# Kernel optimization log

Hardware: AMD Instinct MI355X
Metric: run time of the kernel (lower is better)

The kernel has to match this reference:

```python
import jax, jax.numpy as jnp
import numpy as np

D_MODEL = 1024
N_HEADS = 16
HEAD_DIM = D_MODEL // N_HEADS
D_FF = 4096
EPS = 1e-5


def setup_inputs() -> dict:
    key = jax.random.key(0)
    ks = jax.random.split(key, 12)
    s = 0.02
    return {
        "x": jax.random.normal(ks[0], (2, 2048, D_MODEL), jnp.float32),
        "wq": jax.random.normal(ks[1], (D_MODEL, D_MODEL), jnp.float32) * s,
        "bq": jnp.zeros((D_MODEL,), jnp.float32),
        "wk": jax.random.normal(ks[2], (D_MODEL, D_MODEL), jnp.float32) * s,
        "bk": jnp.zeros((D_MODEL,), jnp.float32),
        "wv": jax.random.normal(ks[3], (D_MODEL, D_MODEL), jnp.float32) * s,
        "bv": jnp.zeros((D_MODEL,), jnp.float32),
        "wo": jax.random.normal(ks[4], (D_MODEL, D_MODEL), jnp.float32) * s,
        "bo": jnp.zeros((D_MODEL,), jnp.float32),
        "w1": jax.random.normal(ks[5], (D_MODEL, D_FF), jnp.float32) * s,
        "b1": jnp.zeros((D_FF,), jnp.float32),
        "w2": jax.random.normal(ks[6], (D_FF, D_MODEL), jnp.float32) * s,
        "b2": jnp.zeros((D_MODEL,), jnp.float32),
        "g1": jnp.ones((D_MODEL,), jnp.float32),
        "be1": jnp.zeros((D_MODEL,), jnp.float32),
        "g2": jnp.ones((D_MODEL,), jnp.float32),
        "be2": jnp.zeros((D_MODEL,), jnp.float32),
    }


def _layer_norm(x, g, b):
    mu = jnp.mean(x, axis=-1, keepdims=True)
    var = jnp.var(x, axis=-1, keepdims=True)
    return (x - mu) * jax.lax.rsqrt(var + EPS) * g + b


def reference(x, wq, bq, wk, bk, wv, bv, wo, bo, w1, b1, w2, b2, g1, be1, g2, be2):
    B, S, D = x.shape
    nx = _layer_norm(x, g1, be1)
    # projections -> [B, H, S, d]
    def split_heads(t):
        return t.reshape(B, S, N_HEADS, HEAD_DIM).transpose(0, 2, 1, 3)
    q = split_heads(nx @ wq + bq)
    k = split_heads(nx @ wk + bk)
    v = split_heads(nx @ wv + bv)
    scores = jnp.einsum("bhqd,bhkd->bhqk", q, k) / jnp.sqrt(jnp.float32(HEAD_DIM))
    attn = jax.nn.softmax(scores, axis=-1)
    out = jnp.einsum("bhqk,bhkd->bhqd", attn, v)
    out = out.transpose(0, 2, 1, 3).reshape(B, S, D)
    x = x + (out @ wo + bo)
    nx = _layer_norm(x, g2, be2)
    ff = jax.nn.relu(nx @ w1 + b1) @ w2 + b2
    return x + ff
```

## Files before the change

kernel.cpp:

```cpp
#include <hip/hip_runtime.h>


typedef __attribute__((ext_vector_type(8))) unsigned short u16x8;
typedef __attribute__((ext_vector_type(4))) unsigned short u16x4;
typedef __attribute__((ext_vector_type(8))) __bf16 bf16x8;
typedef __attribute__((ext_vector_type(4))) float f32x4;

#define C_SCALE 0.1803368801111f

static __device__ __forceinline__ unsigned short f2b(float f) {
    return __builtin_bit_cast(unsigned short, (__bf16)f);
}
static __device__ __forceinline__ float b2f(unsigned short h) {
    unsigned u = ((unsigned)h) << 16;
    float f;
    __builtin_memcpy(&f, &u, 4);
    return f;
}

static __device__ __forceinline__ void async_cp16(
    const unsigned short* g, unsigned short* l)
{
    __builtin_amdgcn_global_load_lds(
        (const __attribute__((address_space(1))) unsigned int*)g,
        (__attribute__((address_space(3))) unsigned int*)l,
        16, 0, 0);
}

__global__ __launch_bounds__(256) void transpose_all_k(
    const float* __restrict__ wq, const float* __restrict__ wk,
    const float* __restrict__ wv, const float* __restrict__ wo,
    const float* __restrict__ w1, const float* __restrict__ w2,
    unsigned short* __restrict__ wqkvT, unsigned short* __restrict__ woT,
    unsigned short* __restrict__ w1T, unsigned short* __restrict__ w2T)
{
    __shared__ unsigned short tile[32][33];
    const int ti = blockIdx.x;
    const float* in;
    unsigned short* out;
    int R, C, bi, bj;
    float sc = 1.0f;
    if (ti < 4096) {
        R = 1024; C = 1024;
        bi = (ti & 1023) >> 5; bj = ti & 31;
        int z = ti >> 10;
        in = (z == 0) ? wq : (z == 1) ? wk : (z == 2) ? wv : wo;
        out = (z < 3) ? wqkvT + (size_t)z * 1024 * 1024 : woT;
        if (z == 1) sc = C_SCALE;
    } else if (ti < 8192) {
        R = 1024; C = 4096;
        int l = ti - 4096;
        bi = l >> 7; bj = l & 127;
        in = w1; out = w1T;
    } else {
        R = 4096; C = 1024;
        int l = ti - 8192;
        bi = l >> 5; bj = l & 31;
        in = w2; out = w2T;
    }
    const int tx = threadIdx.x & 31, ty = threadIdx.x >> 5;
#pragma unroll
    for (int rr = 0; rr < 4; ++rr) {
        int r = ty + rr * 8;
        tile[r][tx] = f2b(in[(size_t)(bi * 32 + r) * C + bj * 32 + tx] * sc);
    }
    __syncthreads();
#pragma unroll
    for (int rr = 0; rr < 4; ++rr) {
        int r = ty + rr * 8;
        out[(size_t)(bj * 32 + r) * R + bi * 32 + tx] = tile[tx][r];
    }
}

__global__ __launch_bounds__(256) void concat3_k(
    const float* __restrict__ a, const float* __restrict__ b,
    const float* __restrict__ c, float* __restrict__ o)
{
    int t = blockIdx.x * 256 + threadIdx.x;
    float v = (t < 1024) ? a[t]
            : ((t < 2048) ? b[t - 1024] * C_SCALE : c[t - 2048]);
    o[t] = v;
}

__global__ __launch_bounds__(256) void ln_kernel(
    const float* __restrict__ x, const float* __restrict__ g,
    const float* __restrict__ be, unsigned short* __restrict__ o)
{
    const int row = blockIdx.x;
    const int t = threadIdx.x;
    const float* xr = x + (size_t)row * 1024;
    float4 v4 = *reinterpret_cast<const float4*>(&xr[t * 4]);
    float f[4] = {v4.x, v4.y, v4.z, v4.w};
    float s = f[0] + f[1] + f[2] + f[3];
    float ss = f[0] * f[0] + f[1] * f[1] + f[2] * f[2] + f[3] * f[3];
#pragma unroll
    for (int d = 1; d < 64; d <<= 1) {
        s += __shfl_xor(s, d);
        ss += __shfl_xor(ss, d);
    }
    __shared__ float sb[4], ssb[4];
    const int wave = t >> 6;
    if ((t & 63) == 0) { sb[wave] = s; ssb[wave] = ss; }
    __syncthreads();
    s = sb[0] + sb[1] + sb[2] + sb[3];
    ss = ssb[0] + ssb[1] + ssb[2] + ssb[3];
    const float mu = s * (1.0f / 1024.0f);
    const float var = ss * (1.0f / 1024.0f) - mu * mu;
    const float rs = rsqrtf(var + 1e-5f);
    u16x4 r4;
#pragma unroll
    for (int j = 0; j < 4; ++j)
        r4[j] = f2b((f[j] - mu) * rs * g[t * 4 + j] + be[t * 4 + j]);
    *reinterpret_cast<u16x4*>(&o[(size_t)row * 1024 + t * 4]) = r4;
}

__global__ __launch_bounds__(256) void reduce_ln_kernel(
    const unsigned short* __restrict__ pa, const unsigned short* __restrict__ pb,
    const float* __restrict__ bias, const float* __restrict__ x,
    const float* __restrict__ g, const float* __restrict__ be,
    float* __restrict__ x2, unsigned short* __restrict__ o)
{
    const int row = blockIdx.x;
    const int t = threadIdx.x;
    const size_t base = (size_t)row * 1024 + t * 4;
    float4 x4 = *reinterpret_cast<const float4*>(&x[base]);
    float4 bb = *reinterpret_cast<const float4*>(&bias[t * 4]);
    float f[4] = {x4.x + bb.x, x4.y + bb.y, x4.z + bb.z, x4.w + bb.w};
#pragma unroll
    for (int z = 0; z < 2; ++z) {
        u16x4 va = *reinterpret_cast<const u16x4*>(&pa[(size_t)z * 4096 * 1024 + base]);
        u16x4 vb = *reinterpret_cast<const u16x4*>(&pb[(size_t)z * 4096 * 1024 + base]);
#pragma unroll
        for (int j = 0; j < 4; ++j) f[j] += b2f(va[j]) + b2f(vb[j]);
    }
    *reinterpret_cast<float4*>(&x2[base]) = {f[0], f[1], f[2], f[3]};
    float s = f[0] + f[1] + f[2] + f[3];
    float ss = f[0] * f[0] + f[1] * f[1] + f[2] * f[2] + f[3] * f[3];
#pragma unroll
    for (int d = 1; d < 64; d <<= 1) {
        s += __shfl_xor(s, d);
        ss += __shfl_xor(ss, d);
    }
    __shared__ float sb[4], ssb[4];
    const int wave = t >> 6;
    if ((t & 63) == 0) { sb[wave] = s; ssb[wave] = ss; }
    __syncthreads();
    s = sb[0] + sb[1] + sb[2] + sb[3];
    ss = ssb[0] + ssb[1] + ssb[2] + ssb[3];
    const float mu = s * (1.0f / 1024.0f);
    const float var = ss * (1.0f / 1024.0f) - mu * mu;
    const float rs = rsqrtf(var + 1e-5f);
    u16x4 r4;
#pragma unroll
    for (int j = 0; j < 4; ++j)
        r4[j] = f2b((f[j] - mu) * rs * g[t * 4 + j] + be[t * 4 + j]);
    *reinterpret_cast<u16x4*>(&o[base]) = r4;
}

__global__ __launch_bounds__(256) void reduce_out4_k(
    const unsigned short* __restrict__ pa, const unsigned short* __restrict__ pb,
    const float* __restrict__ bias, const float* __restrict__ x2,
    float* __restrict__ out)
{
    const size_t i4 = ((size_t)blockIdx.x * 256 + threadIdx.x) * 4;
    float4 x4 = *reinterpret_cast<const float4*>(&x2[i4]);
    float4 bb = *reinterpret_cast<const float4*>(&bias[i4 & 1023]);
    float a0 = x4.x + bb.x, a1 = x4.y + bb.y, a2 = x4.z + bb.z, a3 = x4.w + bb.w;
#pragma unroll
    for (int z = 0; z < 2; ++z) {
        u16x4 va = *reinterpret_cast<const u16x4*>(&pa[(size_t)z * 4096 * 1024 + i4]);
        u16x4 vb = *reinterpret_cast<const u16x4*>(&pb[(size_t)z * 4096 * 1024 + i4]);
        a0 += b2f(va[0]) + b2f(vb[0]);
        a1 += b2f(va[1]) + b2f(vb[1]);
        a2 += b2f(va[2]) + b2f(vb[2]);
        a3 += b2f(va[3]) + b2f(vb[3]);
    }
    *reinterpret_cast<float4*>(&out[i4]) = {a0, a1, a2, a3};
}

template<int MODE, int RELU>
__global__ __launch_bounds__(256, 4) void gemm_bt(
    const unsigned short* __restrict__ A, int lda,
    const unsigned short* __restrict__ Bt, int ldb,
    const float* __restrict__ bias,
    void* __restrict__ Cv, void* __restrict__ Cv2, int N, int Kloop)
{
    __shared__ unsigned short As[128 * 32];
    __shared__ unsigned short Bs[128 * 32];
    const int t = threadIdx.x;
    const int wave = t >> 6, lane = t & 63;
    const int quad = lane >> 4, l16 = lane & 15;
    const int wm = wave >> 1, wn = wave & 1;
    const int m0 = blockIdx.y * 128;
    const int n0 = blockIdx.x * 128;
    const int k0 = blockIdx.z * Kloop;
    const int rl = lane >> 2;
    const int cl = (lane & 3) * 8;

    f32x4 acc[4][4];
#pragma unroll
    for (int mi = 0; mi < 4; ++mi)
#pragma unroll
        for (int ni = 0; ni < 4; ++ni) acc[mi][ni] = {0.f, 0.f, 0.f, 0.f};

    for (int kt = 0; kt < Kloop; kt += 32) {
#pragma unroll
        for (int j = 0; j < 4; ++j) {
            int c = wave * 4 + j;
            if (c < 8) {
                async_cp16(&A[(size_t)(m0 + c * 16 + rl) * lda + k0 + kt + cl],
                           &As[c * 512 + lane * 8]);
            } else {
                int bc = c - 8;
                async_cp16(&Bt[(size_t)(n0 + bc * 16 + rl) * ldb + k0 + kt + cl],
                           &Bs[bc * 512 + lane * 8]);
            }
        }
        __syncthreads();
        bf16x8 af[4], bfr[4];
#pragma unroll
        for (int mi = 0; mi < 4; ++mi)
            af[mi] = __builtin_bit_cast(bf16x8,
                *reinterpret_cast<const u16x8*>(&As[(wm * 64 + mi * 16 + l16) * 32 + quad * 8]));
#pragma unroll
        for (int ni = 0; ni < 4; ++ni)
            bfr[ni] = __builtin_bit_cast(bf16x8,
                *reinterpret_cast<const u16x8*>(&Bs[(wn * 64 + ni * 16 + l16) * 32 + quad * 8]));
#pragma unroll
        for (int mi = 0; mi < 4; ++mi)
#pragma unroll
            for (int ni = 0; ni < 4; ++ni)
                acc[mi][ni] = __builtin_amdgcn_mfma_f32_16x16x32_bf16(
                    af[mi], bfr[ni], acc[mi][ni], 0, 0, 0);
        __syncthreads();
    }

#pragma unroll
    for (int mi = 0; mi < 4; ++mi) {
        const int gr0 = m0 + wm * 64 + mi * 16 + quad * 4;
#pragma unroll
        for (int ni = 0; ni < 4; ++ni) {
            const int gc = n0 + wn * 64 + ni * 16 + l16;
            if (MODE == 2) {
                const float bv = bias[gc];
                if (gc < 2048) {
#pragma unroll
                    for (int r = 0; r < 4; ++r)
                        ((unsigned short*)Cv)[(size_t)(gr0 + r) * 2048 + gc] =
                            f2b(acc[mi][ni][r] + bv);
                } else {
                    u16x4 pk;
#pragma unroll
                    for (int r = 0; r < 4; ++r) pk[r] = f2b(acc[mi][ni][r] + bv);
                    const int b = gr0 >> 11, s0 = gr0 & 2047;
                    *reinterpret_cast<u16x4*>(
                        &((unsigned short*)Cv2)[((size_t)b * 1024 + (gc - 2048)) * 2048 + s0]) = pk;
                }
            } else if (MODE == 5) {
                unsigned short* base = (blockIdx.z < 2)
                    ? (unsigned short*)Cv  + (size_t)blockIdx.z * 4096 * N
                    : (unsigned short*)Cv2 + (size_t)(blockIdx.z - 2) * 4096 * N;
#pragma unroll
                for (int r = 0; r < 4; ++r)
                    base[(size_t)(gr0 + r) * N + gc] = f2b(acc[mi][ni][r]);
            } else {
                const float bv = bias[gc];
#pragma unroll
                for (int r = 0; r < 4; ++r) {
                    float v = acc[mi][ni][r] + bv;
                    if (RELU) v = fmaxf(v, 0.f);
                    ((unsigned short*)Cv)[(size_t)(gr0 + r) * N + gc] = f2b(v);
                }
            }
        }
    }
}

__global__ __launch_bounds__(256, 2) void attn_kernel(
    const unsigned short* __restrict__ qkb, const unsigned short* __restrict__ vbT,
    unsigned short* __restrict__ ao)
{
    __shared__ unsigned short Ks[64][72];
    __shared__ unsigned short Vt[64][72];
    __shared__ unsigned short Ps[4][32][72];
    const int t = threadIdx.x;
    const int wave = t >> 6, lane = t & 63;
    const int quad = lane >> 4, l16 = lane & 15;
    const int bh = blockIdx.y;
    const int b = bh >> 4, h = bh & 15;
    const int q0 = blockIdx.x * 128 + wave * 32;
    const size_t qk_base = (size_t)b * 2048 * 2048;
    const size_t vt_base = (size_t)b * 1024 * 2048 + (size_t)h * 64 * 2048;

    bf16x8 qf[2][2];
#pragma unroll
    for (int m = 0; m < 2; ++m)
#pragma unroll
        for (int kk = 0; kk < 2; ++kk)
            qf[m][kk] = __builtin_bit_cast(bf16x8, *reinterpret_cast<const u16x8*>(
                &qkb[qk_base + (size_t)(q0 + m * 16 + l16) * 2048 + h * 64 + kk * 32 + quad * 8]));

    u16x8 ones_u;
#pragma unroll
    for (int j = 0; j < 8; ++j) ones_u[j] = 0x3F80;
    const bf16x8 onesf = __builtin_bit_cast(bf16x8, ones_u);

    f32x4 o_acc[2][4], l_frag[2];
#pragma unroll
    for (int m = 0; m < 2; ++m) {
        l_frag[m] = {0.f, 0.f, 0.f, 0.f};
#pragma unroll
        for (int nf = 0; nf < 4; ++nf) o_acc[m][nf] = {0.f, 0.f, 0.f, 0.f};
    }

    const int srow0 = t >> 3, sc8 = (t & 7) * 8;
    const int srow1 = srow0 + 32;

    u16x8 kr[2], vr[2];
    kr[0] = *reinterpret_cast<const u16x8*>(&qkb[qk_base + (size_t)srow0 * 2048 + 1024 + h * 64 + sc8]);
    kr[1] = *reinterpret_cast<const u16x8*>(&qkb[qk_base + (size_t)srow1 * 2048 + 1024 + h * 64 + sc8]);
    vr[0] = *reinterpret_cast<const u16x8*>(&vbT[vt_base + (size_t)srow0 * 2048 + sc8]);
    vr[1] = *reinterpret_cast<const u16x8*>(&vbT[vt_base + (size_t)srow1 * 2048 + sc8]);

    for (int it = 0; it < 32; ++it) {
        __syncthreads();
        *reinterpret_cast<u16x8*>(&Ks[srow0][sc8]) = kr[0];
        *reinterpret_cast<u16x8*>(&Ks[srow1][sc8]) = kr[1];
        *reinterpret_cast<u16x8*>(&Vt[srow0][sc8]) = vr[0];
        *reinterpret_cast<u16x8*>(&Vt[srow1][sc8]) = vr[1];
        __syncthreads();
        if (it + 1 < 32) {
            const int ktn = (it + 1) * 64;
            kr[0] = *reinterpret_cast<const u16x8*>(&qkb[qk_base + (size_t)(ktn + srow0) * 2048 + 1024 + h * 64 + sc8]);
            kr[1] = *reinterpret_cast<const u16x8*>(&qkb[qk_base + (size_t)(ktn + srow1) * 2048 + 1024 + h * 64 + sc8]);
            vr[0] = *reinterpret_cast<const u16x8*>(&vbT[vt_base + (size_t)srow0 * 2048 + ktn + sc8]);
            vr[1] = *reinterpret_cast<const u16x8*>(&vbT[vt_base + (size_t)srow1 * 2048 + ktn + sc8]);
        }

#pragma unroll
        for (int kf = 0; kf < 4; ++kf) {
            bf16x8 kfr0 = __builtin_bit_cast(bf16x8,
                *reinterpret_cast<const u16x8*>(&Ks[kf * 16 + l16][quad * 8]));
            bf16x8 kfr1 = __builtin_bit_cast(bf16x8,
                *reinterpret_cast<const u16x8*>(&Ks[kf * 16 + l16][32 + quad * 8]));
#pragma unroll
            for (int m = 0; m < 2; ++m) {
                f32x4 s = {0.f, 0.f, 0.f, 0.f};
                s = __builtin_amdgcn_mfma_f32_16x16x32_bf16(kfr0, qf[m][0], s, 0, 0, 0);
                s = __builtin_amdgcn_mfma_f32_16x16x32_bf16(kfr1, qf[m][1], s, 0, 0, 0);
                unsigned lo = (unsigned)f2b(exp2f(s[0])) | ((unsigned)f2b(exp2f(s[1])) << 16);
                unsigned hi = (unsigned)f2b(exp2f(s[2])) | ((unsigned)f2b(exp2f(s[3])) << 16);
                *reinterpret_cast<uint2*>(&Ps[wave][m * 16 + l16][kf * 16 + quad * 4]) =
                    make_uint2(lo, hi);
            }
        }
#pragma unroll
        for (int kh = 0; kh < 2; ++kh) {
            bf16x8 pfr[2];
#pragma unroll
            for (int m = 0; m < 2; ++m)
                pfr[m] = __builtin_bit_cast(bf16x8,
                    *reinterpret_cast<const u16x8*>(&Ps[wave][m * 16 + l16][kh * 32 + quad * 8]));
#pragma unroll
            for (int m = 0; m < 2; ++m)
                l_frag[m] = __builtin_amdgcn_mfma_f32_16x16x32_bf16(
                    pfr[m], onesf, l_frag[m], 0, 0, 0);
#pragma unroll
            for (int nf = 0; nf < 4; ++nf) {
                bf16x8 vfr = __builtin_bit_cast(bf16x8,
                    *reinterpret_cast<const u16x8*>(&Vt[nf * 16 + l16][kh * 32 + quad * 8]));
#pragma unroll
                for (int m = 0; m < 2; ++m)
                    o_acc[m][nf] = __builtin_amdgcn_mfma_f32_16x16x32_bf16(
                        pfr[m], vfr, o_acc[m][nf], 0, 0, 0);
            }
        }
    }

#pragma unroll
    for (int m = 0; m < 2; ++m) {
#pragma unroll
        for (int r = 0; r < 4; ++r) {
            const float inv = 1.0f / l_frag[m][r];
            const int row = q0 + m * 16 + quad * 4 + r;
#pragma unroll
            for (int nf = 0; nf < 4; ++nf)
                ao[(size_t)b * 2048 * 1024 + (size_t)row * 1024 + h * 64 + nf * 16 + l16] =
                    f2b(o_acc[m][nf][r] * inv);
        }
    }
}

extern "C" void kernel_launch(void* const* d_in, const int* in_sizes, int n_in,
                              void* d_out, int out_size, void* d_ws, size_t ws_size,
                              hipStream_t stream)
{
    const float* x   = (const float*)d_in[0];
    const float* wq  = (const float*)d_in[1];
    const float* bq  = (const float*)d_in[2];
    const float* wk  = (const float*)d_in[3];
    const float* bk  = (const float*)d_in[4];
    const float* wv  = (const float*)d_in[5];
    const float* bv  = (const float*)d_in[6];
    const float* wo  = (const float*)d_in[7];
    const float* bo  = (const float*)d_in[8];
    const float* w1  = (const float*)d_in[9];
    const float* b1  = (const float*)d_in[10];
    const float* w2  = (const float*)d_in[11];
    const float* b2  = (const float*)d_in[12];
    const float* g1  = (const float*)d_in[13];
    const float* be1 = (const float*)d_in[14];
    const float* g2  = (const float*)d_in[15];
    const float* be2 = (const float*)d_in[16];
    float* out = (float*)d_out;
    char*  ws  = (char*)d_ws;

    const int M = 4096, D = 1024, DFF = 4096;
    const size_t MB = 1 << 20;

    unsigned short* wqkvT = (unsigned short*)(ws + 0 * MB);
    unsigned short* woT   = (unsigned short*)(ws + 6 * MB);
    unsigned short* w1T   = (unsigned short*)(ws + 8 * MB);
    unsigned short* w2T   = (unsigned short*)(ws + 16 * MB);
    unsigned short* ln    = (unsigned short*)(ws + 24 * MB);
    unsigned short* qkb   = (unsigned short*)(ws + 32 * MB);
    unsigned short* vbT   = (unsigned short*)(ws + 48 * MB);
    unsigned short* ao    = (unsigned short*)(ws + 56 * MB);
    unsigned short* ff1   = (unsigned short*)(ws + 32 * MB);
    float*          x2    = (float*)(ws + 64 * MB);
    float*          bqkv  = (float*)(ws + 80 * MB);
    unsigned short* pHi   = (unsigned short*)(ws + 80 * MB);
    unsigned short* pOlo  = (unsigned short*)(ws + 32 * MB);
    unsigned short* pFlo  = (unsigned short*)(ws + 0 * MB);

    transpose_all_k<<<12288, 256, 0, stream>>>(wq, wk, wv, wo, w1, w2,
                                               wqkvT, woT, w1T, w2T);
    concat3_k<<<12, 256, 0, stream>>>(bq, bk, bv, bqkv);
    ln_kernel<<<M, 256, 0, stream>>>(x, g1, be1, ln);
    gemm_bt<2, 0><<<dim3(24, 32), 256, 0, stream>>>(
        ln, D, wqkvT, D, bqkv, qkb, vbT, 3072, D);
    attn_kernel<<<dim3(16, 32), 256, 0, stream>>>(qkb, vbT, ao);
    gemm_bt<5, 0><<<dim3(8, 32, 4), 256, 0, stream>>>(
        ao, D, woT, D, nullptr, pHi, pOlo, 1024, 256);
    reduce_ln_kernel<<<M, 256, 0, stream>>>(pHi, pOlo, bo, x, g2, be2, x2, ln);
    gemm_bt<0, 1><<<dim3(32, 32), 256, 0, stream>>>(
        ln, D, w1T, D, b1, ff1, nullptr, DFF, D);
    gemm_bt<5, 0><<<dim3(8, 32, 4), 256, 0, stream>>>(
        ff1, DFF, w2T, DFF, nullptr, pHi, pFlo, 1024, 1024);
    reduce_out4_k<<<4096, 256, 0, stream>>>(pHi, pFlo, b2, x2, out);
}
```

Baseline: 375.5 us.

## Double-buffer K/V tiles and pass P fragments via permlane swaps instead of LDS

The attention kernel now double-buffers the K and V shared-memory tiles and prefetches two tiles ahead, so each iteration needs one barrier instead of two. The softmax probabilities are no longer round-tripped through a per-wave shared buffer. They are rearranged in registers with v_permlane32_swap/v_permlane16_swap, turning the MFMA accumulator layout directly into the A-operand layout for the PV product. This removes LDS traffic and waits on the P path at the cost of more shared memory for K/V, extra live registers, and reliance on gfx950-specific permlane instructions whose lane mapping must be exactly right.

```diff
diff --git a/kernel.cpp b/kernel.cpp
--- a/kernel.cpp
+++ b/kernel.cpp
@@ -5,6 +5,7 @@
 typedef __attribute__((ext_vector_type(4))) unsigned short u16x4;
 typedef __attribute__((ext_vector_type(8))) __bf16 bf16x8;
 typedef __attribute__((ext_vector_type(4))) float f32x4;
+typedef __attribute__((ext_vector_type(4))) unsigned int u32x4;
 
 #define C_SCALE 0.1803368801111f
 
@@ -280,12 +281,12 @@
     const unsigned short* __restrict__ qkb, const unsigned short* __restrict__ vbT,
     unsigned short* __restrict__ ao)
 {
-    __shared__ unsigned short Ks[64][72];
-    __shared__ unsigned short Vt[64][72];
-    __shared__ unsigned short Ps[4][32][72];
+    __shared__ unsigned short Ks[2][64][72];
+    __shared__ unsigned short Vt[2][64][72];
     const int t = threadIdx.x;
-    const int wave = t >> 6, lane = t & 63;
+    const int lane = t & 63;
     const int quad = lane >> 4, l16 = lane & 15;
+    const int wave = t >> 6;
     const int bh = blockIdx.y;
     const int b = bh >> 4, h = bh & 15;
     const int q0 = blockIdx.x * 128 + wave * 32;
@@ -316,65 +317,91 @@
     const int srow0 = t >> 3, sc8 = (t & 7) * 8;
     const int srow1 = srow0 + 32;
 
+    const unsigned short* kg0 = &qkb[qk_base + (size_t)srow0 * 2048 + 1024 + h * 64 + sc8];
+    const unsigned short* kg1 = kg0 + (size_t)32 * 2048;
+    const unsigned short* vg0 = &vbT[vt_base + (size_t)srow0 * 2048 + sc8];
+    const unsigned short* vg1 = vg0 + (size_t)32 * 2048;
+
     u16x8 kr[2], vr[2];
-    kr[0] = *reinterpret_cast<const u16x8*>(&qkb[qk_base + (size_t)srow0 * 2048 + 1024 + h * 64 + sc8]);
-    kr[1] = *reinterpret_cast<const u16x8*>(&qkb[qk_base + (size_t)srow1 * 2048 + 1024 + h * 64 + sc8]);
-    vr[0] = *reinterpret_cast<const u16x8*>(&vbT[vt_base + (size_t)srow0 * 2048 + sc8]);
-    vr[1] = *reinterpret_cast<const u16x8*>(&vbT[vt_base + (size_t)srow1 * 2048 + sc8]);
+    kr[0] = *reinterpret_cast<const u16x8*>(kg0);
+    kr[1] = *reinterpret_cast<const u16x8*>(kg1);
+    vr[0] = *reinterpret_cast<const u16x8*>(vg0);
+    vr[1] = *reinterpret_cast<const u16x8*>(vg1);
+    *reinterpret_cast<u16x8*>(&Ks[0][srow0][sc8]) = kr[0];
+    *reinterpret_cast<u16x8*>(&Ks[0][srow1][sc8]) = kr[1];
+    *reinterpret_cast<u16x8*>(&Vt[0][srow0][sc8]) = vr[0];
+    *reinterpret_cast<u16x8*>(&Vt[0][srow1][sc8]) = vr[1];
+    kr[0] = *reinterpret_cast<const u16x8*>(kg0 + (size_t)64 * 2048);
+    kr[1] = *reinterpret_cast<const u16x8*>(kg1 + (size_t)64 * 2048);
+    vr[0] = *reinterpret_cast<const u16x8*>(vg0 + 64);
+    vr[1] = *reinterpret_cast<const u16x8*>(vg1 + 64);
+    __syncthreads();
 
     for (int it = 0; it < 32; ++it) {
-        __syncthreads();
-        *reinterpret_cast<u16x8*>(&Ks[srow0][sc8]) = kr[0];
-        *reinterpret_cast<u16x8*>(&Ks[srow1][sc8]) = kr[1];
-        *reinterpret_cast<u16x8*>(&Vt[srow0][sc8]) = vr[0];
-        *reinterpret_cast<u16x8*>(&Vt[srow1][sc8]) = vr[1];
-        __syncthreads();
+        const int cur = it & 1, nxt = cur ^ 1;
         if (it + 1 < 32) {
-            const int ktn = (it + 1) * 64;
-            kr[0] = *reinterpret_cast<const u16x8*>(&qkb[qk_base + (size_t)(ktn + srow0) * 2048 + 1024 + h * 64 + sc8]);
-            kr[1] = *reinterpret_cast<const u16x8*>(&qkb[qk_base + (size_t)(ktn + srow1) * 2048 + 1024 + h * 64 + sc8]);
-            vr[0] = *reinterpret_cast<const u16x8*>(&vbT[vt_base + (size_t)srow0 * 2048 + ktn + sc8]);
-            vr[1] = *reinterpret_cast<const u16x8*>(&vbT[vt_base + (size_t)srow1 * 2048 + ktn + sc8]);
-        }
-
-#pragma unroll
-        for (int kf = 0; kf < 4; ++kf) {
-            bf16x8 kfr0 = __builtin_bit_cast(bf16x8,
-                *reinterpret_cast<const u16x8*>(&Ks[kf * 16 + l16][quad * 8]));
-            bf16x8 kfr1 = __builtin_bit_cast(bf16x8,
-                *reinterpret_cast<const u16x8*>(&Ks[kf * 16 + l16][32 + quad * 8]));
+            *reinterpret_cast<u16x8*>(&Ks[nxt][srow0][sc8]) = kr[0];
+            *reinterpret_cast<u16x8*>(&Ks[nxt][srow1][sc8]) = kr[1];
+            *reinterpret_cast<u16x8*>(&Vt[nxt][srow0][sc8]) = vr[0];
+            *reinterpret_cast<u16x8*>(&Vt[nxt][srow1][sc8]) = vr[1];
+        }
+        if (it + 2 < 32) {
+            const size_t ko = (size_t)(it + 2) * 64 * 2048;
+            const int vo = (it + 2) * 64;
+            kr[0] = *reinterpret_cast<const u16x8*>(kg0 + ko);
+            kr[1] = *reinterpret_cast<const u16x8*>(kg1 + ko);
+            vr[0] = *reinterpret_cast<const u16x8*>(vg0 + vo);
+            vr[1] = *reinterpret_cast<const u16x8*>(vg1 + vo);
+        }
+
+#pragma unroll
+        for (int kh = 0; kh < 2; ++kh) {
+            unsigned d0[2][2], d1[2][2];
+#pragma unroll
+            for (int kfi = 0; kfi < 2; ++kfi) {
+                const int kf = kh * 2 + kfi;
+                bf16x8 kfr0 = __builtin_bit_cast(bf16x8,
+                    *reinterpret_cast<const u16x8*>(&Ks[cur][kf * 16 + l16][quad * 8]));
+                bf16x8 kfr1 = __builtin_bit_cast(bf16x8,
+                    *reinterpret_cast<const u16x8*>(&Ks[cur][kf * 16 + l16][32 + quad * 8]));
+#pragma unroll
+                for (int m = 0; m < 2; ++m) {
+                    f32x4 s = {0.f, 0.f, 0.f, 0.f};
+                    s = __builtin_amdgcn_mfma_f32_16x16x32_bf16(kfr0, qf[m][0], s, 0, 0, 0);
+                    s = __builtin_amdgcn_mfma_f32_16x16x32_bf16(kfr1, qf[m][1], s, 0, 0, 0);
+                    d0[m][kfi] = (unsigned)f2b(exp2f(s[0])) |
+                                 ((unsigned)f2b(exp2f(s[1])) << 16);
+                    d1[m][kfi] = (unsigned)f2b(exp2f(s[2])) |
+                                 ((unsigned)f2b(exp2f(s[3])) << 16);
+                }
+            }
+            bf16x8 pfr[2];
 #pragma unroll
             for (int m = 0; m < 2; ++m) {
-                f32x4 s = {0.f, 0.f, 0.f, 0.f};
-                s = __builtin_amdgcn_mfma_f32_16x16x32_bf16(kfr0, qf[m][0], s, 0, 0, 0);
-                s = __builtin_amdgcn_mfma_f32_16x16x32_bf16(kfr1, qf[m][1], s, 0, 0, 0);
-                unsigned lo = (unsigned)f2b(exp2f(s[0])) | ((unsigned)f2b(exp2f(s[1])) << 16);
-                unsigned hi = (unsigned)f2b(exp2f(s[2])) | ((unsigned)f2b(exp2f(s[3])) << 16);
-                *reinterpret_cast<uint2*>(&Ps[wave][m * 16 + l16][kf * 16 + quad * 4]) =
-                    make_uint2(lo, hi);
-            }
-        }
-#pragma unroll
-        for (int kh = 0; kh < 2; ++kh) {
-            bf16x8 pfr[2];
-#pragma unroll
-            for (int m = 0; m < 2; ++m)
-                pfr[m] = __builtin_bit_cast(bf16x8,
-                    *reinterpret_cast<const u16x8*>(&Ps[wave][m * 16 + l16][kh * 32 + quad * 8]));
-#pragma unroll
-            for (int m = 0; m < 2; ++m)
+                unsigned x0 = d0[m][0], y0 = d0[m][1];
+                unsigned x1 = d1[m][0], y1 = d1[m][1];
+                asm("v_permlane32_swap_b32 %0, %1\n\t"
+                    "v_permlane16_swap_b32 %0, %1"
+                    : "+v"(x0), "+v"(y0));
+                asm("v_permlane32_swap_b32 %0, %1\n\t"
+                    "v_permlane16_swap_b32 %0, %1"
+                    : "+v"(x1), "+v"(y1));
+                u32x4 pw = {x0, x1, y0, y1};
+                pfr[m] = __builtin_bit_cast(bf16x8, pw);
                 l_frag[m] = __builtin_amdgcn_mfma_f32_16x16x32_bf16(
                     pfr[m], onesf, l_frag[m], 0, 0, 0);
+            }
 #pragma unroll
             for (int nf = 0; nf < 4; ++nf) {
                 bf16x8 vfr = __builtin_bit_cast(bf16x8,
-                    *reinterpret_cast<const u16x8*>(&Vt[nf * 16 + l16][kh * 32 + quad * 8]));
+                    *reinterpret_cast<const u16x8*>(&Vt[cur][nf * 16 + l16][kh * 32 + quad * 8]));
 #pragma unroll
                 for (int m = 0; m < 2; ++m)
                     o_acc[m][nf] = __builtin_amdgcn_mfma_f32_16x16x32_bf16(
                         pfr[m], vfr, o_acc[m][nf], 0, 0, 0);
             }
         }
+        __syncthreads();
     }
 
 #pragma unroll
```

Result: no change. 381.2 us (+1.5%).
